# Kernel tuning notes

Hardware: AMD Instinct MI355X
Metric: run time of the kernel (lower is better)

## Reference

```python
import jax, jax.numpy as jnp
import numpy as np

B, SQ, SK = 2, 2048, 2048
D_MODEL, N_HEADS = 1024, 16
D_HEAD = D_MODEL // N_HEADS
LN_EPS = 1e-5


def _ln(x, w, b):
    # per-head LayerNorm over last dim (d_head)
    mu = jnp.mean(x, axis=-1, keepdims=True)
    var = jnp.mean(jnp.square(x - mu), axis=-1, keepdims=True)
    return (x - mu) * jax.lax.rsqrt(var + LN_EPS) * w + b


def setup_inputs() -> dict:
    key = jax.random.key(0)
    ks = jax.random.split(key, 8)
    sd = 1.0 / np.sqrt(D_MODEL)
    so = 1.0 / np.sqrt(D_HEAD)
    return {
        "x_q": jax.random.normal(ks[0], (B, SQ, D_MODEL), jnp.float32),
        "x_kv": jax.random.normal(ks[1], (B, SK, D_MODEL), jnp.float32),
        "mask": jnp.tril(jnp.ones((SQ, SK), dtype=bool)),  # causal
        "W_Q": jax.random.normal(ks[2], (N_HEADS, D_MODEL, D_HEAD), jnp.float32) * sd,
        "W_K": jax.random.normal(ks[3], (N_HEADS, D_MODEL, D_HEAD), jnp.float32) * sd,
        "W_V": jax.random.normal(ks[4], (N_HEADS, D_MODEL, D_HEAD), jnp.float32) * sd,
        "W_O": jax.random.normal(ks[5], (N_HEADS, D_HEAD, D_MODEL), jnp.float32) * so,
        "b_Q": jnp.zeros((N_HEADS, D_HEAD), jnp.float32),
        "b_K": jnp.zeros((N_HEADS, D_HEAD), jnp.float32),
        "b_V": jnp.zeros((N_HEADS, D_HEAD), jnp.float32),
        "b_O": jnp.zeros((D_MODEL,), jnp.float32),
        "ln1_w": jnp.ones((D_HEAD,), jnp.float32),
        "ln1_b": jnp.zeros((D_HEAD,), jnp.float32),
        "ln2_w": jnp.ones((D_HEAD,), jnp.float32),
        "ln2_b": jnp.zeros((D_HEAD,), jnp.float32),
    }


def reference(x_q, x_kv, mask, W_Q, W_K, W_V, W_O, b_Q, b_K, b_V, b_O,
              ln1_w, ln1_b, ln2_w, ln2_b):
    # QKV projections: b s d, n d h -> b s n h
    q = jnp.einsum('bsd,ndh->bsnh', x_q, W_Q) + b_Q
    k = jnp.einsum('bsd,ndh->bsnh', x_kv, W_K) + b_K
    v = jnp.einsum('bsd,ndh->bsnh', x_kv, W_V) + b_V
    # QK-norm (ln_first=False, rope=None -> just apply LN after projections)
    q = _ln(q, ln1_w, ln1_b)
    k = _ln(k, ln2_w, ln2_b)
    # NOTE: no 1/sqrt(d_head) scaling, matching the original module
    att = jnp.einsum('bqnh,bknh->bnqk', q, k)
    att = jnp.where(mask, att, -jnp.inf)
    probas = jax.nn.softmax(att, axis=-1)
    z = jnp.einsum('bnqk,bknh->bqnh', probas, v)
    out = jnp.einsum('bqnh,nhd->bqd', z, W_O) + b_O
    return (out, k, v)
```

## Files before the change

kernel.cpp:

```cpp
#include <hip/hip_runtime.h>
#include <hip/hip_bf16.h>

#define B_   2
#define SQ_  2048
#define DM_  1024
#define NH_  16
#define DH_  64

typedef __attribute__((ext_vector_type(8))) short          bf16x8;
typedef __attribute__((ext_vector_type(4))) short          bf16x4;
typedef __attribute__((ext_vector_type(8))) unsigned short u16x8;
typedef __attribute__((ext_vector_type(4))) float          f32x4;

__device__ __forceinline__ unsigned short f2bf(float f) {
    union { __hip_bfloat16 h; unsigned short u; } c;
    c.h = __float2bfloat16(f);
    return c.u;
}
__device__ __forceinline__ float gsum16(float v) {
    v += __shfl_xor(v, 1);
    v += __shfl_xor(v, 2);
    v += __shfl_xor(v, 4);
    v += __shfl_xor(v, 8);
    return v;
}

__device__ __forceinline__ f32x4 mfma16(bf16x4 a, bf16x4 b, f32x4 c) {
#if __has_builtin(__builtin_amdgcn_mfma_f32_16x16x16bf16_1k)
    return __builtin_amdgcn_mfma_f32_16x16x16bf16_1k(a, b, c, 0, 0, 0);
#else
    asm("v_mfma_f32_16x16x16_bf16 %0, %1, %2, %0" : "+v"(c) : "v"(a), "v"(b));
    return c;
#endif
}

template <int N> __device__ __forceinline__ void waitv() {
    if constexpr (N == 0)      asm volatile("s_waitcnt vmcnt(0)" ::: "memory");
    else if constexpr (N == 2) asm volatile("s_waitcnt vmcnt(2)" ::: "memory");
    else if constexpr (N == 3) asm volatile("s_waitcnt vmcnt(3)" ::: "memory");
    else if constexpr (N == 4) asm volatile("s_waitcnt vmcnt(4)" ::: "memory");
    else if constexpr (N == 6) asm volatile("s_waitcnt vmcnt(6)" ::: "memory");
}

__device__ __forceinline__ void gll16(const unsigned short* g, unsigned short* l) {
    __builtin_amdgcn_global_load_lds(
        (const __attribute__((address_space(1))) unsigned int*)g,
        (__attribute__((address_space(3))) unsigned int*)l,
        16, 0, 0);
}

__global__ __launch_bounds__(256) void prep_all(
    const float* __restrict__ W_Q, const float* __restrict__ W_K,
    const float* __restrict__ W_V, const float* __restrict__ W_O,
    const float* __restrict__ x_q, const float* __restrict__ x_kv,
    unsigned short* __restrict__ WTq, unsigned short* __restrict__ WTkv,
    unsigned short* __restrict__ WTo,
    unsigned short* __restrict__ xqbf, unsigned short* __restrict__ xkvbf)
{
    const int bid = blockIdx.x, tid = threadIdx.x;
    if (bid >= 1024) {
        const int cid = bid - 1024;
        const float* src = (cid < 512) ? x_q : x_kv;
        unsigned short* dst = (cid < 512) ? xqbf : xkvbf;
        const size_t base = (size_t)(cid & 511) * 8192 + tid * 4;
#pragma unroll
        for (int i = 0; i < 8; ++i) {
            const float4 v = *(const float4*)(src + base + i * 1024);
            ushort4 o;
            o.x = f2bf(v.x); o.y = f2bf(v.y); o.z = f2bf(v.z); o.w = f2bf(v.w);
            *(ushort4*)(dst + base + i * 1024) = o;
        }
        return;
    }
    __shared__ float t[64][65];
    const float* src; unsigned short* dst; int R, C, r0, c0;
    if (bid < 768) {
        const int which = bid >> 8, rem = bid & 255;
        const int rblk = rem & 15, zz = rem >> 4;
        src = (which == 0) ? W_Q : (which == 1) ? W_K : W_V;
        dst = (which == 0) ? WTq : (which == 1) ? WTkv : (WTkv + (1u << 20));
        src += (size_t)65536 * zz;
        dst += (size_t)65536 * zz;
        R = 1024; C = 64; r0 = rblk * 64; c0 = 0;
    } else {
        const int rem = bid - 768;
        src = W_O; dst = WTo; R = 1024; C = 1024;
        r0 = (rem & 15) * 64; c0 = (rem >> 4) * 64;
    }
    const int lr = tid >> 6, lc = tid & 63;
#pragma unroll
    for (int i = 0; i < 16; ++i)
        t[lr + i * 4][lc] = src[(size_t)(r0 + lr + i * 4) * C + c0 + lc];
    __syncthreads();
    const int u = tid & 15, w0 = tid >> 4;
#pragma unroll
    for (int i = 0; i < 4; ++i) {
        const int cl = w0 + i * 16;
        ushort4 o;
        o.x = f2bf(t[4 * u + 0][cl]);
        o.y = f2bf(t[4 * u + 1][cl]);
        o.z = f2bf(t[4 * u + 2][cl]);
        o.w = f2bf(t[4 * u + 3][cl]);
        *(ushort4*)&dst[(size_t)(c0 + cl) * R + r0 + 4 * u] = o;
    }
}

template <int TM, int MODE, int NT>
__device__ __forceinline__ void gemm_body(
    unsigned short* __restrict__ As,
    unsigned short* __restrict__ Bs,
    int bx, int by, const unsigned short* __restrict__ Abf,
    const unsigned short* __restrict__ WT,
    const float* __restrict__ biasK, const float* __restrict__ biasV,
    const float* __restrict__ lnw, const float* __restrict__ lnb,
    float* __restrict__ Cf, float* __restrict__ Cf2,
    unsigned short* __restrict__ Cb, unsigned short* __restrict__ CbT, int tid)
{
    constexpr int NW    = NT / 64;
    constexpr int WROWS = 2 * TM / NW;
    constexpr int MI    = WROWS / 16;
    constexpr int RP    = NT / 8;
    constexpr int APASS = TM / RP;
    constexpr int BPASS = 128 / RP;
    constexpr int LOADS = APASS + BPASS;

    const int m0 = by * TM;
    const int c0 = bx * 128;

    const int wid = tid >> 6, lane = tid & 63;
    const int wm = (wid >> 1) * WROWS;
    const int wn = (wid & 1) * 64;
    const int l15 = lane & 15, qd = lane >> 4;

    const int srow  = tid >> 3;
    const int pslot = tid & 7;
    const int sslot = pslot ^ (srow & 7);
    const unsigned short* Ag = Abf + (size_t)(m0 + srow) * 1024 + sslot * 8;
    const unsigned short* Bg = WT  + (size_t)(c0 + srow) * 1024 + sslot * 8;
    unsigned short* Al = As + srow * 64 + pslot * 8;
    unsigned short* Bl = Bs + srow * 64 + pslot * 8;

    const f32x4 zero4 = {0.f, 0.f, 0.f, 0.f};
    f32x4 acc[MI][4];
#pragma unroll
    for (int mi = 0; mi < MI; ++mi)
#pragma unroll
        for (int ni = 0; ni < 4; ++ni) acc[mi][ni] = zero4;

    const int r7 = l15 & 7;

#define STAGE(kb_, bi_)                                                        \
    {                                                                          \
        const size_t kof_ = (size_t)(kb_) * 64;                                \
        _Pragma("unroll")                                                      \
        for (int j = 0; j < APASS; ++j)                                        \
            gll16(Ag + (size_t)j * RP * 1024 + kof_,                           \
                  Al + (bi_) * (TM * 64) + j * RP * 64);                       \
        _Pragma("unroll")                                                      \
        for (int j = 0; j < BPASS; ++j)                                        \
            gll16(Bg + (size_t)j * RP * 1024 + kof_,                           \
                  Bl + (bi_) * (128 * 64) + j * RP * 64);                      \
    }

    STAGE(0, 0)
    for (int kb = 0; kb < 16; ++kb) {
        const int cur = kb & 1;
        if (kb < 15) {
            STAGE(kb + 1, cur ^ 1)
            waitv<LOADS>();
        } else {
            waitv<0>();
        }
        __builtin_amdgcn_sched_barrier(0);
        __builtin_amdgcn_s_barrier();
        __builtin_amdgcn_sched_barrier(0);
#pragma unroll
        for (int ks = 0; ks < 2; ++ks) {
            const int cs = ((ks * 4 + qd) ^ r7) * 8;
            bf16x8 af[MI], bfr[4];
#pragma unroll
            for (int mi = 0; mi < MI; ++mi)
                af[mi] = *(const bf16x8*)(As + cur * (TM * 64) +
                                          (wm + mi * 16 + l15) * 64 + cs);
#pragma unroll
            for (int ni = 0; ni < 4; ++ni)
                bfr[ni] = *(const bf16x8*)(Bs + cur * (128 * 64) +
                                           (wn + ni * 16 + l15) * 64 + cs);
#pragma unroll
            for (int mi = 0; mi < MI; ++mi)
#pragma unroll
                for (int ni = 0; ni < 4; ++ni)
                    acc[mi][ni] = __builtin_amdgcn_mfma_f32_16x16x32_bf16(
                        af[mi], bfr[ni], acc[mi][ni], 0, 0, 0);
        }
        __builtin_amdgcn_sched_barrier(0);
        __builtin_amdgcn_s_barrier();
    }
#undef STAGE

    const float* bias = (MODE == 1 && c0 >= 1024) ? biasV : biasK;
    float bv[4];
#pragma unroll
    for (int ni = 0; ni < 4; ++ni) bv[ni] = bias[(c0 + wn + ni * 16 + l15) & 1023];
#pragma unroll
    for (int mi = 0; mi < MI; ++mi)
#pragma unroll
        for (int ni = 0; ni < 4; ++ni)
#pragma unroll
            for (int r = 0; r < 4; ++r) acc[mi][ni][r] += bv[ni];

    if constexpr (MODE != 2) {
        const bool doLN = (MODE == 0) || (c0 < 1024);
        if (doLN) {
            float w4[4], lb4[4];
#pragma unroll
            for (int ni = 0; ni < 4; ++ni) {
                w4[ni]  = lnw[ni * 16 + l15];
                lb4[ni] = lnb[ni * 16 + l15];
            }
#pragma unroll
            for (int mi = 0; mi < MI; ++mi)
#pragma unroll
                for (int r = 0; r < 4; ++r) {
                    float s1 = acc[mi][0][r] + acc[mi][1][r] + acc[mi][2][r] + acc[mi][3][r];
                    const float mu = gsum16(s1) * (1.0f / 64.0f);
                    float s2 = acc[mi][0][r] * acc[mi][0][r] + acc[mi][1][r] * acc[mi][1][r]
                             + acc[mi][2][r] * acc[mi][2][r] + acc[mi][3][r] * acc[mi][3][r];
                    const float var = gsum16(s2) * (1.0f / 64.0f) - mu * mu;
                    const float rstd = rsqrtf(var + 1e-5f);
#pragma unroll
                    for (int ni = 0; ni < 4; ++ni)
                        acc[mi][ni][r] = (acc[mi][ni][r] - mu) * rstd * w4[ni] + lb4[ni];
                }
        }
    }

    if constexpr (MODE == 0) {
#pragma unroll
        for (int mi = 0; mi < MI; ++mi)
#pragma unroll
            for (int r = 0; r < 4; ++r) {
                const size_t grow = m0 + wm + mi * 16 + qd * 4 + r;
#pragma unroll
                for (int ni = 0; ni < 4; ++ni)
                    Cb[grow * 1024 + c0 + wn + ni * 16 + l15] = f2bf(acc[mi][ni][r]);
            }
    } else if constexpr (MODE == 2) {
#pragma unroll
        for (int mi = 0; mi < MI; ++mi)
#pragma unroll
            for (int r = 0; r < 4; ++r) {
                const size_t grow = m0 + wm + mi * 16 + qd * 4 + r;
#pragma unroll
                for (int ni = 0; ni < 4; ++ni)
                    Cf[grow * 1024 + c0 + wn + ni * 16 + l15] = acc[mi][ni][r];
            }
    } else {
        if (c0 < 1024) {
#pragma unroll
            for (int mi = 0; mi < MI; ++mi)
#pragma unroll
                for (int r = 0; r < 4; ++r) {
                    const size_t grow = m0 + wm + mi * 16 + qd * 4 + r;
#pragma unroll
                    for (int ni = 0; ni < 4; ++ni) {
                        const int gcol = c0 + wn + ni * 16 + l15;
                        Cf[grow * 1024 + gcol] = acc[mi][ni][r];
                        Cb[grow * 1024 + gcol] = f2bf(acc[mi][ni][r]);
                    }
                }
        } else {
#pragma unroll
            for (int mi = 0; mi < MI; ++mi) {
                const int growb = m0 + wm + mi * 16 + qd * 4;
                const int bb_ = growb >> 11, ss = growb & 2047;
#pragma unroll
                for (int ni = 0; ni < 4; ++ni) {
                    const int gv = c0 - 1024 + wn + ni * 16 + l15;
                    const int hh = gv >> 6, dd = gv & 63;
#pragma unroll
                    for (int r = 0; r < 4; ++r)
                        Cf2[(size_t)(growb + r) * 1024 + gv] = acc[mi][ni][r];
                    ushort4 w;
                    w.x = f2bf(acc[mi][ni][0]); w.y = f2bf(acc[mi][ni][1]);
                    w.z = f2bf(acc[mi][ni][2]); w.w = f2bf(acc[mi][ni][3]);
                    *(ushort4*)&CbT[(((size_t)bb_ * NH_ + hh) * DH_ + dd) * SQ_ + ss] = w;
                }
            }
        }
    }
}

__global__ __launch_bounds__(512) void qkv_fused(
    const unsigned short* __restrict__ xqbf, const unsigned short* __restrict__ xkvbf,
    const unsigned short* __restrict__ WTq, const unsigned short* __restrict__ WTkv,
    const float* __restrict__ b_Q, const float* __restrict__ b_K,
    const float* __restrict__ b_V,
    const float* __restrict__ ln1w, const float* __restrict__ ln1b,
    const float* __restrict__ ln2w, const float* __restrict__ ln2b,
    float* __restrict__ kout, float* __restrict__ vout,
    unsigned short* __restrict__ qz, unsigned short* __restrict__ kbf,
    unsigned short* __restrict__ vbfT)
{
    __shared__ __align__(16) unsigned short As[2 * 64 * 64];
    __shared__ __align__(16) unsigned short Bs[2 * 128 * 64];
    const int bid = blockIdx.x, tid = threadIdx.x;
    if (bid < 1024) {
        gemm_body<64, 1, 512>(As, Bs, bid & 15, bid >> 4, xkvbf, WTkv, b_K, b_V,
                              ln2w, ln2b, kout, vout, kbf, vbfT, tid);
    } else {
        const int b2 = bid - 1024;
        gemm_body<64, 0, 512>(As, Bs, b2 & 7, b2 >> 3, xqbf, WTq, b_Q, nullptr,
                              ln1w, ln1b, nullptr, nullptr, qz, nullptr, tid);
    }
}

__global__ __launch_bounds__(512) void o_gemm(
    const unsigned short* __restrict__ zbf, const unsigned short* __restrict__ WTo,
    const float* __restrict__ b_O, float* __restrict__ out)
{
    __shared__ __align__(16) unsigned short As[2 * 64 * 64];
    __shared__ __align__(16) unsigned short Bs[2 * 128 * 64];
    gemm_body<64, 2, 512>(As, Bs, blockIdx.x, blockIdx.y, zbf, WTo, b_O, nullptr,
                          nullptr, nullptr, out, nullptr, nullptr, nullptr,
                          threadIdx.x);
}

__global__ __launch_bounds__(512) void attn_mfma(
    unsigned short* __restrict__ qz, const unsigned short* __restrict__ kbf,
    const unsigned short* __restrict__ vbfT)
{
    __shared__ __align__(16) unsigned short Ks[2][128][72];
    __shared__ __align__(16) unsigned short VsT[2][64][136];

    const int tid = threadIdx.x;
    const int h = blockIdx.y, b = blockIdx.z;
    const int wid = tid >> 6, lane = tid & 63;
    const int g = wid & 3, p = wid >> 2;
    const int l15 = lane & 15, qd = lane >> 4;
    const int srow = tid >> 2, scol = (tid & 3) * 16;
    const int vrow = tid >> 3, vcol = (tid & 7) * 16;

    const size_t kbase = (size_t)b * SQ_ * DM_ + (size_t)h * DH_;
    const size_t vbase = ((size_t)b * NH_ + h) * DH_ * (size_t)SQ_;
    const f32x4 zero4 = {0.f, 0.f, 0.f, 0.f};
    const float LOG2E = 1.44269504f, MBIAS = 46.1662413f;

    float* zs = (float*)&Ks[0][0][0];
    float* ls = (float*)&VsT[0][0][0];

    for (int pass = 0; pass < 2; ++pass) {
        const int qt = pass ? blockIdx.x : 31 - blockIdx.x;

        bf16x8 qf[2];
        {
            const unsigned short* qp =
                qz + kbase + (size_t)(qt * 64 + g * 16 + l15) * DM_ + qd * 8;
            qf[0] = *(const bf16x8*)(qp);
            qf[1] = *(const bf16x8*)(qp + 32);
        }

        f32x4 z[4];
#pragma unroll
        for (int ni = 0; ni < 4; ++ni) z[ni] = zero4;
        float l_i = 0.f;

        {
            const unsigned short* ks = kbf + kbase + (size_t)srow * DM_ + scol;
            const u16x8 a0 = *(const u16x8*)(ks);
            const u16x8 a1 = *(const u16x8*)(ks + 8);
            const unsigned short* vs = vbfT + vbase + (size_t)vrow * SQ_ + vcol;
            const u16x8 b0 = *(const u16x8*)(vs);
            const u16x8 b1 = *(const u16x8*)(vs + 8);
            *(u16x8*)&Ks[0][srow][scol + 0]  = a0;
            *(u16x8*)&Ks[0][srow][scol + 8]  = a1;
            *(u16x8*)&VsT[0][vrow][vcol + 0] = b0;
            *(u16x8*)&VsT[0][vrow][vcol + 8] = b1;
        }
        __syncthreads();

        const int NS = (qt >> 1) + 1;
        for (int st = 0; st < NS; ++st) {
            const int cur = st & 1;

            u16x8 kr0, kr1, vr0, vr1;
            if (st < NS - 1) {
                const unsigned short* ks =
                    kbf + kbase + (size_t)((st + 1) * 128 + srow) * DM_ + scol;
                kr0 = *(const u16x8*)(ks);
                kr1 = *(const u16x8*)(ks + 8);
                const unsigned short* vs =
                    vbfT + vbase + (size_t)vrow * SQ_ + (st + 1) * 128 + vcol;
                vr0 = *(const u16x8*)(vs);
                vr1 = *(const u16x8*)(vs + 8);
            }

            const int kt = st * 2 + p;
            if (kt <= qt) {
                f32x4 s[4];
#pragma unroll
                for (int mi = 0; mi < 4; ++mi) s[mi] = zero4;
#pragma unroll
                for (int ks2 = 0; ks2 < 2; ++ks2)
#pragma unroll
                    for (int mi = 0; mi < 4; ++mi) {
                        const bf16x8 af = *(const bf16x8*)
                            &Ks[cur][p * 64 + mi * 16 + l15][ks2 * 32 + qd * 8];
                        s[mi] = __builtin_amdgcn_mfma_f32_16x16x32_bf16(
                            af, qf[ks2], s[mi], 0, 0, 0);
                    }

                if (kt == qt) {
#pragma unroll
                    for (int mi = 0; mi < 4; ++mi)
#pragma unroll
                        for (int r = 0; r < 4; ++r)
                            if (mi * 16 + qd * 4 + r > g * 16 + l15)
                                s[mi][r] = -3.0e38f;
                }

                float ts[4];
                bf16x4 pa[4];
#pragma unroll
                for (int mi = 0; mi < 4; ++mi) {
#pragma unroll
                    for (int r = 0; r < 4; ++r)
                        s[mi][r] = __builtin_amdgcn_exp2f(
                            fmaf(s[mi][r], LOG2E, -MBIAS));
                    ts[mi] = (s[mi][0] + s[mi][1]) + (s[mi][2] + s[mi][3]);
                    pa[mi][0] = (short)f2bf(s[mi][0]);
                    pa[mi][1] = (short)f2bf(s[mi][1]);
                    pa[mi][2] = (short)f2bf(s[mi][2]);
                    pa[mi][3] = (short)f2bf(s[mi][3]);
                }
                float rs = (ts[0] + ts[1]) + (ts[2] + ts[3]);
                rs += __shfl_xor(rs, 16);
                rs += __shfl_xor(rs, 32);
                l_i += rs;

#pragma unroll
                for (int mi = 0; mi < 4; ++mi)
#pragma unroll
                    for (int ni = 0; ni < 4; ++ni) {
                        const bf16x4 bv = *(const bf16x4*)
                            &VsT[cur][ni * 16 + l15][p * 64 + mi * 16 + qd * 4];
                        z[ni] = mfma16(pa[mi], bv, z[ni]);
                    }
            }

            if (st < NS - 1) {
                *(u16x8*)&Ks[cur ^ 1][srow][scol + 0]  = kr0;
                *(u16x8*)&Ks[cur ^ 1][srow][scol + 8]  = kr1;
                *(u16x8*)&VsT[cur ^ 1][vrow][vcol + 0] = vr0;
                *(u16x8*)&VsT[cur ^ 1][vrow][vcol + 8] = vr1;
            }
            __syncthreads();
        }

        if (p == 1) {
#pragma unroll
            for (int ni = 0; ni < 4; ++ni)
                *(f32x4*)&zs[((g * 4 + ni) * 64 + lane) * 4] = z[ni];
            ls[g * 64 + lane] = l_i;
        }
        __syncthreads();
        if (p == 0) {
            const float l_tot = l_i + ls[g * 64 + lane];
#pragma unroll
            for (int ni = 0; ni < 4; ++ni) {
                const f32x4 zo = *(const f32x4*)&zs[((g * 4 + ni) * 64 + lane) * 4];
#pragma unroll
                for (int r = 0; r < 4; ++r) z[ni][r] += zo[r];
            }
            const float linv = 1.0f / l_tot;
#pragma unroll
            for (int r = 0; r < 4; ++r) {
                const float lr_ = __shfl(linv, qd * 4 + r);
                const size_t row = (size_t)qt * 64 + g * 16 + qd * 4 + r;
#pragma unroll
                for (int ni = 0; ni < 4; ++ni)
                    qz[kbase + row * DM_ + ni * 16 + l15] = f2bf(z[ni][r] * lr_);
            }
        }
        __syncthreads();
    }
}

extern "C" void kernel_launch(void* const* d_in, const int* in_sizes, int n_in,
                              void* d_out, int out_size, void* d_ws, size_t ws_size,
                              hipStream_t stream)
{
    const float* x_q  = (const float*)d_in[0];
    const float* x_kv = (const float*)d_in[1];
    const float* W_Q  = (const float*)d_in[3];
    const float* W_K  = (const float*)d_in[4];
    const float* W_V  = (const float*)d_in[5];
    const float* W_O  = (const float*)d_in[6];
    const float* b_Q  = (const float*)d_in[7];
    const float* b_K  = (const float*)d_in[8];
    const float* b_V  = (const float*)d_in[9];
    const float* b_O  = (const float*)d_in[10];
    const float* ln1w = (const float*)d_in[11];
    const float* ln1b = (const float*)d_in[12];
    const float* ln2w = (const float*)d_in[13];
    const float* ln2b = (const float*)d_in[14];

    const size_t NTOK = (size_t)B_ * SQ_;
    float* out  = (float*)d_out;
    float* kout = out + NTOK * DM_;
    float* vout = kout + NTOK * DM_;

    unsigned short* xqbf  = (unsigned short*)out;
    unsigned short* xkvbf = xqbf + (1u << 22);

    unsigned short* wsu  = (unsigned short*)d_ws;
    unsigned short* WTq  = wsu;
    unsigned short* WTkv = WTq + (1u << 20);
    unsigned short* WTo  = WTkv + (2u << 20);
    unsigned short* qz   = WTo + (1u << 20);
    unsigned short* kbf  = qz + (1u << 22);
    unsigned short* vbfT = kbf + (1u << 22);

    prep_all<<<2048, 256, 0, stream>>>(W_Q, W_K, W_V, W_O, x_q, x_kv,
                                       WTq, WTkv, WTo, xqbf, xkvbf);

    qkv_fused<<<1536, 512, 0, stream>>>(xqbf, xkvbf, WTq, WTkv, b_Q, b_K, b_V,
                                        ln1w, ln1b, ln2w, ln2b,
                                        kout, vout, qz, kbf, vbfT);

    attn_mfma<<<dim3(16, NH_, B_), 512, 0, stream>>>(qz, kbf, vbfT);

    o_gemm<<<dim3(8, 64), 512, 0, stream>>>(qz, WTo, b_O, out);
}
```

Measured before the change: 225.9 us.

## Process paired causal query tiles in one K/V sweep in attention kernel

The attention kernel used to handle its two query tiles (low and high) in two passes, each streaming K/V from global memory. It now keeps both tiles' Q fragments and accumulators live together and streams K/V once, applying each staged tile to both query tiles while the low tile is still in range. This removes the second pass's K/V reloads and its separate prologue. The extra live registers are partly offset by a launch-bounds hint asking for 4 blocks per CU, which risks register spills.

```diff
diff --git a/kernel.cpp b/kernel.cpp
--- a/kernel.cpp
+++ b/kernel.cpp
@@ -326,7 +326,7 @@
                           threadIdx.x);
 }
 
-__global__ __launch_bounds__(512) void attn_mfma(
+__global__ __launch_bounds__(512, 4) void attn_mfma(
     unsigned short* __restrict__ qz, const unsigned short* __restrict__ kbf,
     const unsigned short* __restrict__ vbfT)
 {
@@ -349,141 +349,155 @@
     float* zs = (float*)&Ks[0][0][0];
     float* ls = (float*)&VsT[0][0][0];
 
-    for (int pass = 0; pass < 2; ++pass) {
-        const int qt = pass ? blockIdx.x : 31 - blockIdx.x;
-
-        bf16x8 qf[2];
-        {
-            const unsigned short* qp =
-                qz + kbase + (size_t)(qt * 64 + g * 16 + l15) * DM_ + qd * 8;
-            qf[0] = *(const bf16x8*)(qp);
-            qf[1] = *(const bf16x8*)(qp + 32);
-        }
-
-        f32x4 z[4];
-#pragma unroll
-        for (int ni = 0; ni < 4; ++ni) z[ni] = zero4;
-        float l_i = 0.f;
-
-        {
-            const unsigned short* ks = kbf + kbase + (size_t)srow * DM_ + scol;
-            const u16x8 a0 = *(const u16x8*)(ks);
-            const u16x8 a1 = *(const u16x8*)(ks + 8);
-            const unsigned short* vs = vbfT + vbase + (size_t)vrow * SQ_ + vcol;
-            const u16x8 b0 = *(const u16x8*)(vs);
-            const u16x8 b1 = *(const u16x8*)(vs + 8);
-            *(u16x8*)&Ks[0][srow][scol + 0]  = a0;
-            *(u16x8*)&Ks[0][srow][scol + 8]  = a1;
-            *(u16x8*)&VsT[0][vrow][vcol + 0] = b0;
-            *(u16x8*)&VsT[0][vrow][vcol + 8] = b1;
+    const int qt_lo = blockIdx.x;
+    const int qt_hi = 31 - qt_lo;
+
+    bf16x8 qfl[2], qfh[2];
+    {
+        const unsigned short* ql =
+            qz + kbase + (size_t)(qt_lo * 64 + g * 16 + l15) * DM_ + qd * 8;
+        qfl[0] = *(const bf16x8*)(ql);
+        qfl[1] = *(const bf16x8*)(ql + 32);
+        const unsigned short* qh =
+            qz + kbase + (size_t)(qt_hi * 64 + g * 16 + l15) * DM_ + qd * 8;
+        qfh[0] = *(const bf16x8*)(qh);
+        qfh[1] = *(const bf16x8*)(qh + 32);
+    }
+
+    f32x4 zl[4], zh[4];
+#pragma unroll
+    for (int ni = 0; ni < 4; ++ni) { zl[ni] = zero4; zh[ni] = zero4; }
+    float ll = 0.f, lh = 0.f;
+
+    {
+        const unsigned short* ks = kbf + kbase + (size_t)srow * DM_ + scol;
+        const u16x8 a0 = *(const u16x8*)(ks);
+        const u16x8 a1 = *(const u16x8*)(ks + 8);
+        const unsigned short* vs = vbfT + vbase + (size_t)vrow * SQ_ + vcol;
+        const u16x8 b0 = *(const u16x8*)(vs);
+        const u16x8 b1 = *(const u16x8*)(vs + 8);
+        *(u16x8*)&Ks[0][srow][scol + 0]  = a0;
+        *(u16x8*)&Ks[0][srow][scol + 8]  = a1;
+        *(u16x8*)&VsT[0][vrow][vcol + 0] = b0;
+        *(u16x8*)&VsT[0][vrow][vcol + 8] = b1;
+    }
+    __syncthreads();
+
+#define TILE_STEP(qf_, z_, l_, qt_)                                            \
+    {                                                                          \
+        f32x4 s[4];                                                            \
+        _Pragma("unroll")                                                      \
+        for (int mi = 0; mi < 4; ++mi) s[mi] = zero4;                          \
+        _Pragma("unroll")                                                      \
+        for (int ks2 = 0; ks2 < 2; ++ks2)                                      \
+            _Pragma("unroll")                                                  \
+            for (int mi = 0; mi < 4; ++mi) {                                   \
+                const bf16x8 af = *(const bf16x8*)                             \
+                    &Ks[cur][p * 64 + mi * 16 + l15][ks2 * 32 + qd * 8];       \
+                s[mi] = __builtin_amdgcn_mfma_f32_16x16x32_bf16(               \
+                    af, qf_[ks2], s[mi], 0, 0, 0);                             \
+            }                                                                  \
+        if (kt == (qt_)) {                                                     \
+            _Pragma("unroll")                                                  \
+            for (int mi = 0; mi < 4; ++mi)                                     \
+                _Pragma("unroll")                                              \
+                for (int r = 0; r < 4; ++r)                                    \
+                    if (mi * 16 + qd * 4 + r > g * 16 + l15)                   \
+                        s[mi][r] = -3.0e38f;                                   \
+        }                                                                      \
+        float ts[4];                                                           \
+        bf16x4 pa[4];                                                          \
+        _Pragma("unroll")                                                      \
+        for (int mi = 0; mi < 4; ++mi) {                                       \
+            _Pragma("unroll")                                                  \
+            for (int r = 0; r < 4; ++r)                                        \
+                s[mi][r] = __builtin_amdgcn_exp2f(                             \
+                    fmaf(s[mi][r], LOG2E, -MBIAS));                            \
+            ts[mi] = (s[mi][0] + s[mi][1]) + (s[mi][2] + s[mi][3]);            \
+            pa[mi][0] = (short)f2bf(s[mi][0]);                                 \
+            pa[mi][1] = (short)f2bf(s[mi][1]);                                 \
+            pa[mi][2] = (short)f2bf(s[mi][2]);                                 \
+            pa[mi][3] = (short)f2bf(s[mi][3]);                                 \
+        }                                                                      \
+        float rs = (ts[0] + ts[1]) + (ts[2] + ts[3]);                          \
+        rs += __shfl_xor(rs, 16);                                              \
+        rs += __shfl_xor(rs, 32);                                              \
+        l_ += rs;                                                              \
+        _Pragma("unroll")                                                      \
+        for (int mi = 0; mi < 4; ++mi)                                         \
+            _Pragma("unroll")                                                  \
+            for (int ni = 0; ni < 4; ++ni) {                                   \
+                const bf16x4 bv = *(const bf16x4*)                             \
+                    &VsT[cur][ni * 16 + l15][p * 64 + mi * 16 + qd * 4];       \
+                z_[ni] = mfma16(pa[mi], bv, z_[ni]);                           \
+            }                                                                  \
+    }
+
+    const int NS = (qt_hi >> 1) + 1;
+    for (int st = 0; st < NS; ++st) {
+        const int cur = st & 1;
+
+        u16x8 kr0, kr1, vr0, vr1;
+        if (st < NS - 1) {
+            const unsigned short* ks =
+                kbf + kbase + (size_t)((st + 1) * 128 + srow) * DM_ + scol;
+            kr0 = *(const u16x8*)(ks);
+            kr1 = *(const u16x8*)(ks + 8);
+            const unsigned short* vs =
+                vbfT + vbase + (size_t)vrow * SQ_ + (st + 1) * 128 + vcol;
+            vr0 = *(const u16x8*)(vs);
+            vr1 = *(const u16x8*)(vs + 8);
+        }
+
+        const int kt = st * 2 + p;
+        if (kt <= qt_hi) TILE_STEP(qfh, zh, lh, qt_hi)
+        if (kt <= qt_lo) TILE_STEP(qfl, zl, ll, qt_lo)
+
+        if (st < NS - 1) {
+            *(u16x8*)&Ks[cur ^ 1][srow][scol + 0]  = kr0;
+            *(u16x8*)&Ks[cur ^ 1][srow][scol + 8]  = kr1;
+            *(u16x8*)&VsT[cur ^ 1][vrow][vcol + 0] = vr0;
+            *(u16x8*)&VsT[cur ^ 1][vrow][vcol + 8] = vr1;
         }
         __syncthreads();
-
-        const int NS = (qt >> 1) + 1;
-        for (int st = 0; st < NS; ++st) {
-            const int cur = st & 1;
-
-            u16x8 kr0, kr1, vr0, vr1;
-            if (st < NS - 1) {
-                const unsigned short* ks =
-                    kbf + kbase + (size_t)((st + 1) * 128 + srow) * DM_ + scol;
-                kr0 = *(const u16x8*)(ks);
-                kr1 = *(const u16x8*)(ks + 8);
-                const unsigned short* vs =
-                    vbfT + vbase + (size_t)vrow * SQ_ + (st + 1) * 128 + vcol;
-                vr0 = *(const u16x8*)(vs);
-                vr1 = *(const u16x8*)(vs + 8);
-            }
-
-            const int kt = st * 2 + p;
-            if (kt <= qt) {
-                f32x4 s[4];
-#pragma unroll
-                for (int mi = 0; mi < 4; ++mi) s[mi] = zero4;
-#pragma unroll
-                for (int ks2 = 0; ks2 < 2; ++ks2)
-#pragma unroll
-                    for (int mi = 0; mi < 4; ++mi) {
-                        const bf16x8 af = *(const bf16x8*)
-                            &Ks[cur][p * 64 + mi * 16 + l15][ks2 * 32 + qd * 8];
-                        s[mi] = __builtin_amdgcn_mfma_f32_16x16x32_bf16(
-                            af, qf[ks2], s[mi], 0, 0, 0);
-                    }
-
-                if (kt == qt) {
-#pragma unroll
-                    for (int mi = 0; mi < 4; ++mi)
-#pragma unroll
-                        for (int r = 0; r < 4; ++r)
-                            if (mi * 16 + qd * 4 + r > g * 16 + l15)
-                                s[mi][r] = -3.0e38f;
-                }
-
-                float ts[4];
-                bf16x4 pa[4];
-#pragma unroll
-                for (int mi = 0; mi < 4; ++mi) {
-#pragma unroll
-                    for (int r = 0; r < 4; ++r)
-                        s[mi][r] = __builtin_amdgcn_exp2f(
-                            fmaf(s[mi][r], LOG2E, -MBIAS));
-                    ts[mi] = (s[mi][0] + s[mi][1]) + (s[mi][2] + s[mi][3]);
-                    pa[mi][0] = (short)f2bf(s[mi][0]);
-                    pa[mi][1] = (short)f2bf(s[mi][1]);
-                    pa[mi][2] = (short)f2bf(s[mi][2]);
-                    pa[mi][3] = (short)f2bf(s[mi][3]);
-                }
-                float rs = (ts[0] + ts[1]) + (ts[2] + ts[3]);
-                rs += __shfl_xor(rs, 16);
-                rs += __shfl_xor(rs, 32);
-                l_i += rs;
-
-#pragma unroll
-                for (int mi = 0; mi < 4; ++mi)
-#pragma unroll
-                    for (int ni = 0; ni < 4; ++ni) {
-                        const bf16x4 bv = *(const bf16x4*)
-                            &VsT[cur][ni * 16 + l15][p * 64 + mi * 16 + qd * 4];
-                        z[ni] = mfma16(pa[mi], bv, z[ni]);
-                    }
-            }
-
-            if (st < NS - 1) {
-                *(u16x8*)&Ks[cur ^ 1][srow][scol + 0]  = kr0;
-                *(u16x8*)&Ks[cur ^ 1][srow][scol + 8]  = kr1;
-                *(u16x8*)&VsT[cur ^ 1][vrow][vcol + 0] = vr0;
-                *(u16x8*)&VsT[cur ^ 1][vrow][vcol + 8] = vr1;
-            }
-            __syncthreads();
-        }
-
-        if (p == 1) {
-#pragma unroll
-            for (int ni = 0; ni < 4; ++ni)
-                *(f32x4*)&zs[((g * 4 + ni) * 64 + lane) * 4] = z[ni];
-            ls[g * 64 + lane] = l_i;
-        }
-        __syncthreads();
-        if (p == 0) {
-            const float l_tot = l_i + ls[g * 64 + lane];
-#pragma unroll
-            for (int ni = 0; ni < 4; ++ni) {
-                const f32x4 zo = *(const f32x4*)&zs[((g * 4 + ni) * 64 + lane) * 4];
-#pragma unroll
-                for (int r = 0; r < 4; ++r) z[ni][r] += zo[r];
-            }
-            const float linv = 1.0f / l_tot;
-#pragma unroll
-            for (int r = 0; r < 4; ++r) {
-                const float lr_ = __shfl(linv, qd * 4 + r);
-                const size_t row = (size_t)qt * 64 + g * 16 + qd * 4 + r;
-#pragma unroll
-                for (int ni = 0; ni < 4; ++ni)
-                    qz[kbase + row * DM_ + ni * 16 + l15] = f2bf(z[ni][r] * lr_);
-            }
-        }
-        __syncthreads();
-    }
+    }
+#undef TILE_STEP
+
+#define COMBINE(z_, l_, qt_)                                                   \
+    {                                                                          \
+        if (p == 1) {                                                          \
+            _Pragma("unroll")                                                  \
+            for (int ni = 0; ni < 4; ++ni)                                     \
+                *(f32x4*)&zs[((g * 4 + ni) * 64 + lane) * 4] = z_[ni];         \
+            ls[g * 64 + lane] = l_;                                            \
+        }                                                                      \
+        __syncthreads();                                                       \
+        if (p == 0) {                                                          \
+            const float l_tot = l_ + ls[g * 64 + lane];                        \
+            _Pragma("unroll")                                                  \
+            for (int ni = 0; ni < 4; ++ni) {                                   \
+                const f32x4 zo =                                               \
+                    *(const f32x4*)&zs[((g * 4 + ni) * 64 + lane) * 4];        \
+                _Pragma("unroll")                                              \
+                for (int r = 0; r < 4; ++r) z_[ni][r] += zo[r];                \
+            }                                                                  \
+            const float linv = 1.0f / l_tot;                                   \
+            _Pragma("unroll")                                                  \
+            for (int r = 0; r < 4; ++r) {                                      \
+                const float lr_ = __shfl(linv, qd * 4 + r);                    \
+                const size_t row = (size_t)(qt_) * 64 + g * 16 + qd * 4 + r;   \
+                _Pragma("unroll")                                              \
+                for (int ni = 0; ni < 4; ++ni)                                 \
+                    qz[kbase + row * DM_ + ni * 16 + l15] =                    \
+                        f2bf(z_[ni][r] * lr_);                                 \
+            }                                                                  \
+        }                                                                      \
+    }
+
+    COMBINE(zh, lh, qt_hi)
+    __syncthreads();
+    COMBINE(zl, ll, qt_lo)
+#undef COMBINE
 }
 
 extern "C" void kernel_launch(void* const* d_in, const int* in_sizes, int n_in,
```

Result: no change. 228.6 us (+1.2%).
